# Kernel tuning notes

Measured on AMD Instinct MI355X. Metric: run time of the kernel, lower is better.

The kernel has to match this reference:

```python
import jax, jax.numpy as jnp
import numpy as np

B, N, NODE_DIM = 256, 200, 2
H, D, L, FF = 8, 128, 3, 512
KD = D // H  # key/val dim per head = 16
EPS = 1e-5


def _uniform(key, shape, fan):
    s = 1.0 / np.sqrt(fan)
    return jax.random.uniform(key, shape, jnp.float32, -s, s)


def setup_inputs() -> dict:
    key = jax.random.key(0)
    ks = jax.random.split(key, 16)
    return {
        "x": jax.random.normal(ks[0], (B, N, NODE_DIM), jnp.float32),
        "Wemb": _uniform(ks[1], (NODE_DIM, D), NODE_DIM),
        "bemb": _uniform(ks[2], (D,), NODE_DIM),
        "Wq": _uniform(ks[3], (L, H, D, KD), KD),
        "Wk": _uniform(ks[4], (L, H, D, KD), KD),
        "Wv": _uniform(ks[5], (L, H, D, KD), KD),
        "Wo": _uniform(ks[6], (L, H, KD, D), D),
        "bn1_g": jnp.ones((L, D), jnp.float32),
        "bn1_b": jnp.zeros((L, D), jnp.float32),
        "W1": _uniform(ks[7], (L, D, FF), D),
        "b1": _uniform(ks[8], (L, FF), D),
        "W2": _uniform(ks[9], (L, FF, D), FF),
        "b2": _uniform(ks[10], (L, D), FF),
        "bn2_g": jnp.ones((L, D), jnp.float32),
        "bn2_b": jnp.zeros((L, D), jnp.float32),
    }


def _batch_norm(h, g, b):
    # BatchNorm1d in training mode: stats over all (batch*graph) positions per channel
    hf = h.reshape(-1, h.shape[-1])
    m = hf.mean(axis=0)
    v = hf.var(axis=0)  # biased variance, as torch uses for normalization
    return (h - m) * jax.lax.rsqrt(v + EPS) * g + b


def _mha(h, Wq, Wk, Wv, Wo):
    # h: [B,N,D]; Wq/Wk/Wv: [H,D,KD]; Wo: [H,KD,D]
    Q = jnp.einsum('bnd,hdk->hbnk', h, Wq)
    K = jnp.einsum('bnd,hdk->hbnk', h, Wk)
    V = jnp.einsum('bnd,hdk->hbnk', h, Wv)
    scores = jnp.einsum('hbqk,hbnk->hbqn', Q, K) * (1.0 / np.sqrt(KD))
    attn = jax.nn.softmax(scores, axis=-1)
    heads = jnp.einsum('hbqn,hbnk->hbqk', attn, V)
    return jnp.einsum('hbqk,hkd->bqd', heads, Wo)


def reference(x, Wemb, bemb, Wq, Wk, Wv, Wo, bn1_g, bn1_b, W1, b1, W2, b2, bn2_g, bn2_b):
    h = x @ Wemb + bemb  # init_embed: [B,N,D]
    for l in range(L):
        h = h + _mha(h, Wq[l], Wk[l], Wv[l], Wo[l])
        h = _batch_norm(h, bn1_g[l], bn1_b[l])
        ff = jax.nn.relu(h @ W1[l] + b1[l]) @ W2[l] + b2[l]
        h = _batch_norm(h + ff, bn2_g[l], bn2_b[l])
    return (h, h.mean(axis=1))
```

## Files before the change

kernel.cpp:

```cpp
#include <hip/hip_runtime.h>
#include <math.h>

#define B_ 256
#define N_ 200
#define D_ 128
#define H_ 8
#define KD_ 16
#define L_ 3
#define FF_ 512
#define ROWS (B_*N_)
#define BND (ROWS*D_)

typedef float f32x4 __attribute__((ext_vector_type(4)));
typedef _Float16 f16x4 __attribute__((ext_vector_type(4)));
typedef _Float16 f16x8 __attribute__((ext_vector_type(8)));

__device__ __forceinline__ ushort f2h_bits(float f) {
  _Float16 h = (_Float16)f;
  union { _Float16 h; ushort u; } v; v.h = h; return v.u;
}
__device__ __forceinline__ float h2f(ushort u) {
  union { ushort u; _Float16 h; } v; v.u = u; return (float)v.h;
}
__device__ __forceinline__ void splith(float f, ushort& hi, ushort& lo) {
  _Float16 h = (_Float16)f;
  float hf = (float)h;
  _Float16 l = (_Float16)(f - hf);
  union { _Float16 h; ushort u; } a, b; a.h = h; b.h = l;
  hi = a.u; lo = b.u;
}
__device__ __forceinline__ void bn_reduce(const float* psum, const float* psq,
    const float* gamma, const float* beta, int c, float& sc, float& sh) {
  if (gamma == nullptr) { sc = 1.f; sh = 0.f; return; }
  float s = 0.f, q = 0.f;
  for (int r = 0; r < 400; r++) { s += psum[r*128 + c]; q += psq[r*128 + c]; }
  const float invM = 1.f / 51200.f;
  float m = s * invM;
  float v = fmaf(q, invM, -m * m);
  float rr = rsqrtf(v + 1e-5f);
  sc = rr * gamma[c];
  sh = fmaf(-m, sc, beta[c]);
}

__global__ __launch_bounds__(256) void embed_kernel(const float* __restrict__ x,
    const float* __restrict__ Wemb, const float* __restrict__ bemb,
    ushort* __restrict__ hhi, ushort* __restrict__ hlo)
{
  int i4 = blockIdx.x * 256 + threadIdx.x;
  int r  = i4 >> 5, c4 = i4 & 31;
  float x0 = x[2*r], x1 = x[2*r + 1];
  const float4 w0 = ((const float4*)Wemb)[c4];
  const float4 w1 = ((const float4*)Wemb)[32 + c4];
  const float4 bb = ((const float4*)bemb)[c4];
  float o[4];
  o[0] = fmaf(x0, w0.x, fmaf(x1, w1.x, bb.x));
  o[1] = fmaf(x0, w0.y, fmaf(x1, w1.y, bb.y));
  o[2] = fmaf(x0, w0.z, fmaf(x1, w1.z, bb.z));
  o[3] = fmaf(x0, w0.w, fmaf(x1, w1.w, bb.w));
  ushort hi[4], lo[4];
#pragma unroll
  for (int k = 0; k < 4; k++) splith(o[k], hi[k], lo[k]);
  uint2 ph, pl;
  ph.x = (uint)hi[0] | ((uint)hi[1] << 16);
  ph.y = (uint)hi[2] | ((uint)hi[3] << 16);
  pl.x = (uint)lo[0] | ((uint)lo[1] << 16);
  pl.y = (uint)lo[2] | ((uint)lo[3] << 16);
  ((uint2*)hhi)[i4] = ph;
  ((uint2*)hlo)[i4] = pl;
}

__global__ __launch_bounds__(256) void t_weights(const float* __restrict__ Wo,
    const float* __restrict__ W2, ushort* __restrict__ woT, ushort* __restrict__ w2T)
{
  int i = blockIdx.x * 256 + threadIdx.x;
  if (i < 49152) {
    int l = i / 16384, r = i % 16384;
    int n = r >> 7, k = r & 127;
    int hh = k >> 4, kd = k & 15;
    woT[i] = f2h_bits(Wo[l*16384 + hh*2048 + kd*128 + n]);
  } else {
    int j = i - 49152;
    int l = j / 65536, r = j % 65536;
    int d = r >> 9, f = r & 511;
    w2T[j] = f2h_bits(W2[l*65536 + f*128 + d]);
  }
}

__global__ __launch_bounds__(128) void fold_qkv(const float* __restrict__ Wq,
    const float* __restrict__ Wk, const float* __restrict__ Wv,
    const float* __restrict__ psum, const float* __restrict__ psq,
    const float* __restrict__ gamma, const float* __restrict__ beta,
    ushort* __restrict__ wh, float* __restrict__ bout,
    float* __restrict__ scout, float* __restrict__ shout)
{
  __shared__ float wsum[2];
  int n = blockIdx.x;
  int k = threadIdx.x;
  float sc, sh;
  bn_reduce(psum, psq, gamma, beta, k, sc, sh);
  if (n == 0) { scout[k] = sc; shout[k] = sh; }
  int which = n >> 7, hh = (n >> 4) & 7, kd = n & 15;
  const float* src = (which == 0) ? Wq : (which == 1) ? Wk : Wv;
  float w = src[hh*2048 + k*16 + kd];
  if (which == 0) w *= 0.25f * 1.44269504088896340736f;
  wh[n*128 + k] = f2h_bits(w * sc);
  float p = sh * w;
#pragma unroll
  for (int d = 1; d < 64; d <<= 1) p += __shfl_xor(p, d);
  if ((k & 63) == 0) wsum[k >> 6] = p;
  __syncthreads();
  if (k == 0) bout[n] = wsum[0] + wsum[1];
}

__global__ __launch_bounds__(128) void fold_w1(const float* __restrict__ W1,
    const float* __restrict__ b1,
    const float* __restrict__ psum, const float* __restrict__ psq,
    const float* __restrict__ gamma, const float* __restrict__ beta,
    ushort* __restrict__ wh, float* __restrict__ bout,
    float* __restrict__ scout, float* __restrict__ shout)
{
  __shared__ float wsum[2];
  int f = blockIdx.x;
  int k = threadIdx.x;
  float sc, sh;
  bn_reduce(psum, psq, gamma, beta, k, sc, sh);
  if (f == 0) { scout[k] = sc; shout[k] = sh; }
  float w = W1[k*512 + f];
  wh[f*128 + k] = f2h_bits(w * sc);
  float p = sh * w;
#pragma unroll
  for (int d = 1; d < 64; d <<= 1) p += __shfl_xor(p, d);
  if ((k & 63) == 0) wsum[k >> 6] = p;
  __syncthreads();
  if (k == 0) bout[f] = b1[f] + wsum[0] + wsum[1];
}

template<int K, bool BIAS, bool RELU, bool RESIDBN,
         bool OUTQKV, bool OUT16, bool OUTHL, bool STATS>
__global__ __launch_bounds__(256, 2) void gemm_mfma(
    const ushort* __restrict__ Ah,
    const ushort* __restrict__ Wh,
    const float* __restrict__ bias,
    const ushort* rhi, const ushort* rlo,
    const float* __restrict__ rsc, const float* __restrict__ rsh,
    ushort* o0, ushort* o1, ushort* o2,
    float* __restrict__ psum, float* __restrict__ psq, int Ntot)
{
  __shared__ ushort AhS[128*64];
  __shared__ ushort BhS[128*64];
  const int t    = threadIdx.x;
  const int nx   = gridDim.x;
  const int nwg  = nx * gridDim.y;
  const int lin  = blockIdx.y * nx + blockIdx.x;
  const int q8   = nwg >> 3, r8 = nwg & 7;
  const int xcd  = lin & 7, i8 = lin >> 3;
  const int wg   = (xcd < r8 ? xcd*(q8+1) : r8*(q8+1) + (xcd-r8)*q8) + i8;
  const int bm   = (wg / nx) * 128;
  const int bn   = (wg % nx) * 128;
  const int lane = t & 63;
  const int w    = t >> 6, wm = w >> 1, wn = w & 1;
  const int quad = lane >> 4, l15 = lane & 15;
  const int bky  = wg / nx;

  f32x4 acc[4][4];
#pragma unroll
  for (int i = 0; i < 4; i++)
#pragma unroll
    for (int j = 0; j < 4; j++) acc[i][j] = (f32x4){0.f, 0.f, 0.f, 0.f};

  const ushort* AhB = Ah + (size_t)bm * K;
  const ushort* BhB = Wh + (size_t)bn * K;

  for (int k0 = 0; k0 < K; k0 += 64) {
#pragma unroll
    for (int i = 0; i < 4; i++) {
      int idx = i * 256 + t;
      int row = idx >> 3, c = idx & 7;
      int k8  = c ^ (row & 7);
      size_t off = (size_t)row * K + k0 + k8 * 8;
      ((uint4*)AhS)[idx] = *(const uint4*)(AhB + off);
      ((uint4*)BhS)[idx] = *(const uint4*)(BhB + off);
    }
    __syncthreads();
#pragma unroll
    for (int ks = 0; ks < 2; ks++) {
      f16x8 ah[4], bh[4];
#pragma unroll
      for (int i = 0; i < 4; i++) {
        int row = wm * 64 + i * 16 + l15;
        int k8  = ks * 4 + quad;
        int ci  = k8 ^ (row & 7);
        ah[i] = ((const f16x8*)AhS)[row * 8 + ci];
        int nrow = wn * 64 + i * 16 + l15;
        int cj   = k8 ^ (nrow & 7);
        bh[i] = ((const f16x8*)BhS)[nrow * 8 + cj];
      }
#pragma unroll
      for (int i = 0; i < 4; i++)
#pragma unroll
        for (int j = 0; j < 4; j++)
          acc[i][j] = __builtin_amdgcn_mfma_f32_16x16x32_f16(ah[i], bh[j], acc[i][j], 0, 0, 0);
    }
    __syncthreads();
  }

  float bv[4], scv[4], shv[4];
#pragma unroll
  for (int j = 0; j < 4; j++) {
    int col = bn + wn*64 + j*16 + l15;
    if (BIAS)    bv[j]  = bias[col];
    if (RESIDBN) { scv[j] = rsc[col]; shv[j] = rsh[col]; }
  }
  float sj[4] = {0.f,0.f,0.f,0.f}, qj[4] = {0.f,0.f,0.f,0.f};
#pragma unroll
  for (int i = 0; i < 4; i++) {
#pragma unroll
    for (int r = 0; r < 4; r++) {
      int row = bm + wm*64 + i*16 + quad*4 + r;
#pragma unroll
      for (int j = 0; j < 4; j++) {
        int col = bn + wn*64 + j*16 + l15;
        float v = acc[i][j][r];
        if (BIAS)    v += bv[j];
        if (RELU)    v = fmaxf(v, 0.f);
        if (RESIDBN) {
          size_t ri = (size_t)row * Ntot + col;
          float rr = h2f(rhi[ri]) + h2f(rlo[ri]);
          v += fmaf(rr, scv[j], shv[j]);
        }
        if (OUTQKV) {
          if (bn == 0) {
            o0[((size_t)(col >> 4) * ROWS + row) * 16 + (col & 15)] = f2h_bits(v);
          } else if (bn == 128) {
            int c = col - 128;
            o1[((size_t)(c >> 4) * ROWS + row) * 16 + (c & 15)] = f2h_bits(v);
          } else {
            int c = col - 256;
            o2[((size_t)(c >> 4) * ROWS + row) * 16 + (c & 15)] = f2h_bits(v);
          }
        }
        if (OUT16) o0[(size_t)row * Ntot + col] = f2h_bits(v);
        if (OUTHL) {
          ushort hi, lo; splith(v, hi, lo);
          o0[(size_t)row * Ntot + col] = hi;
          o1[(size_t)row * Ntot + col] = lo;
        }
        if (STATS) { sj[j] += v; qj[j] = fmaf(v, v, qj[j]); }
      }
    }
  }
  if (STATS) {
#pragma unroll
    for (int j = 0; j < 4; j++) {
      sj[j] += __shfl_xor(sj[j], 16); sj[j] += __shfl_xor(sj[j], 32);
      qj[j] += __shfl_xor(qj[j], 16); qj[j] += __shfl_xor(qj[j], 32);
    }
    float* ssum = (float*)AhS;
    float* ssq  = ssum + 128;
    if (t < 128) { ssum[t] = 0.f; ssq[t] = 0.f; }
    __syncthreads();
    if (quad == 0) {
#pragma unroll
      for (int j = 0; j < 4; j++) {
        int col = wn*64 + j*16 + l15;
        atomicAdd(&ssum[col], sj[j]);
        atomicAdd(&ssq[col],  qj[j]);
      }
    }
    __syncthreads();
    if (t < 128) {
      psum[bky * 128 + t] = ssum[t];
      psq [bky * 128 + t] = ssq[t];
    }
  }
}

__global__ __launch_bounds__(256) void attn_kernel(const ushort* __restrict__ qs,
    const ushort* __restrict__ ks, const ushort* __restrict__ vh,
    ushort* __restrict__ hd)
{
  __shared__ __align__(16) _Float16 Ksh[208*24];
  __shared__ __align__(16) _Float16 VTh[16*216];
  const int b  = blockIdx.x >> 3;
  const int hh = blockIdx.x & 7;
  const int t  = threadIdx.x;
  const size_t rb = (size_t)b * N_;
  const size_t hb = ((size_t)hh * ROWS + rb) * 16;

  for (int i = t; i < 208*2; i += 256) {
    int n = i >> 1, half = i & 1;
    uint4 kv = {0u, 0u, 0u, 0u};
    if (n < N_) kv = *(const uint4*)(ks + hb + n*16 + half*8);
    *(uint4*)&Ksh[n*24 + half*8] = kv;
  }
  for (int i = t; i < 208*2; i += 256) {
    int n = i >> 1, half = i & 1;
    uint4 v0 = {0u, 0u, 0u, 0u};
    if (n < N_) v0 = *(const uint4*)(vh + hb + n*16 + half*8);
    const ushort* e0 = (const ushort*)&v0;
#pragma unroll
    for (int q = 0; q < 8; q++)
      ((ushort*)VTh)[(half*8 + q)*216 + n] = e0[q];
  }
  __syncthreads();

  const int lane = t & 63;
  const int w    = t >> 6;
  const int l15  = lane & 15;
  const int g    = lane >> 4;

  for (int qt = w; qt < 13; qt += 4) {
    int qr  = qt*16 + l15;
    int qrc = qr < N_ ? qr : N_-1;
    f16x4 bq = *(const f16x4*)(qs + hb + (size_t)qrc*16 + g*4);

    f32x4 ct[13];
#pragma unroll
    for (int kt = 0; kt < 13; kt++) {
      f16x4 ak = *(const f16x4*)&Ksh[(kt*16 + l15)*24 + g*4];
      ct[kt] = __builtin_amdgcn_mfma_f32_16x16x16f16(ak, bq, (f32x4){0.f,0.f,0.f,0.f}, 0, 0, 0);
    }
#pragma unroll
    for (int r = 0; r < 4; r++)
      if (g*4 + r >= 8) ct[12][r] = -1e30f;

    float m0 = -1e30f, m1 = -1e30f;
#pragma unroll
    for (int kt = 0; kt < 13; kt++) {
      m0 = fmaxf(m0, fmaxf(ct[kt][0], ct[kt][1]));
      m1 = fmaxf(m1, fmaxf(ct[kt][2], ct[kt][3]));
    }
    float m = fmaxf(m0, m1);
    m = fmaxf(m, __shfl_xor(m, 16));
    m = fmaxf(m, __shfl_xor(m, 32));

    float la0 = 0.f, la1 = 0.f, la2 = 0.f, la3 = 0.f;
#pragma unroll
    for (int kt = 0; kt < 13; kt++) {
      float p0 = __builtin_amdgcn_exp2f(ct[kt][0] - m);
      float p1 = __builtin_amdgcn_exp2f(ct[kt][1] - m);
      float p2 = __builtin_amdgcn_exp2f(ct[kt][2] - m);
      float p3 = __builtin_amdgcn_exp2f(ct[kt][3] - m);
      la0 += p0; la1 += p1; la2 += p2; la3 += p3;
      ct[kt][0] = p0; ct[kt][1] = p1; ct[kt][2] = p2; ct[kt][3] = p3;
    }
    float l = (la0 + la1) + (la2 + la3);
    l += __shfl_xor(l, 16);
    l += __shfl_xor(l, 32);

    f32x4 och = {0.f,0.f,0.f,0.f};
#pragma unroll
    for (int kt = 0; kt < 13; kt++) {
      f16x4 pt = { (_Float16)ct[kt][0], (_Float16)ct[kt][1],
                   (_Float16)ct[kt][2], (_Float16)ct[kt][3] };
      f16x4 avh = *(const f16x4*)&VTh[l15*216 + kt*16 + g*4];
      och = __builtin_amdgcn_mfma_f32_16x16x16f16(avh, pt, och, 0, 0, 0);
    }

    if (qr < N_) {
      float inv = __builtin_amdgcn_rcpf(l);
      ushort o16[4];
#pragma unroll
      for (int r = 0; r < 4; r++) o16[r] = f2h_bits(och[r] * inv);
      uint2 p;
      p.x = (uint)o16[0] | ((uint)o16[1] << 16);
      p.y = (uint)o16[2] | ((uint)o16[3] << 16);
      *(uint2*)(hd + (rb + qr)*128 + hh*16 + g*4) = p;
    }
  }
}

__global__ __launch_bounds__(256) void bn_mean_final(const ushort* __restrict__ hhi,
    const ushort* __restrict__ hlo,
    const float* __restrict__ psum, const float* __restrict__ psq,
    const float* __restrict__ gamma, const float* __restrict__ beta,
    float* __restrict__ outh, float* __restrict__ mout)
{
  __shared__ float part[2][128];
  int b = blockIdx.x;
  int t = threadIdx.x;
  int d = t & 127, half = t >> 7;
  float sc, sh;
  bn_reduce(psum, psq, gamma, beta, d, sc, sh);
  float s = 0.f;
  for (int n = half*100; n < half*100 + 100; n++) {
    size_t idx = ((size_t)b * N_ + n) * 128 + d;
    float v = fmaf(h2f(hhi[idx]) + h2f(hlo[idx]), sc, sh);
    outh[idx] = v;
    s += v;
  }
  part[half][d] = s;
  __syncthreads();
  if (half == 0) mout[b * 128 + d] = (part[0][d] + part[1][d]) * (1.f / N_);
}

extern "C" void kernel_launch(void* const* d_in, const int* in_sizes, int n_in,
                              void* d_out, int out_size, void* d_ws, size_t ws_size,
                              hipStream_t stream)
{
  const float* x    = (const float*)d_in[0];
  const float* Wemb = (const float*)d_in[1];
  const float* bemb = (const float*)d_in[2];
  const float* Wq   = (const float*)d_in[3];
  const float* Wk   = (const float*)d_in[4];
  const float* Wv   = (const float*)d_in[5];
  const float* Wo   = (const float*)d_in[6];
  const float* bn1g = (const float*)d_in[7];
  const float* bn1b = (const float*)d_in[8];
  const float* W1   = (const float*)d_in[9];
  const float* b1   = (const float*)d_in[10];
  const float* W2   = (const float*)d_in[11];
  const float* b2   = (const float*)d_in[12];
  const float* bn2g = (const float*)d_in[13];
  const float* bn2b = (const float*)d_in[14];
  float* out = (float*)d_out;

  char* wsb = (char*)d_ws;
  ushort* h_hi  = (ushort*)wsb;
  ushort* h_lo  = (ushort*)(wsb + 13107200);
  char*   phase = wsb + 26214400;
  ushort* qsb   = (ushort*)phase;
  ushort* ksb   = (ushort*)(phase + 13107200);
  ushort* vhh   = (ushort*)(phase + 26214400);
  ushort* hd    = (ushort*)(phase + 52428800);
  ushort* hid   = (ushort*)phase;
  char*   wp    = wsb + 91750400;
  ushort* woT   = (ushort*)wp;
  ushort* w2T   = (ushort*)(wp + 98304);
  ushort* fqkvw = (ushort*)(wp + 491520);
  ushort* fw1w  = (ushort*)(wp + 589824);
  float*  fqkv_b = (float*)(wp + 720896);
  float*  fw1_b  = (float*)(wp + 722432);
  float*  psum   = (float*)(wp + 724480);
  float*  psq    = (float*)(wp + 929280);
  float*  sc_a   = (float*)(wp + 1134080);
  float*  sh_a   = (float*)(wp + 1134592);
  float*  sc_b   = (float*)(wp + 1135104);
  float*  sh_b   = (float*)(wp + 1135616);

  embed_kernel<<<6400, 256, 0, stream>>>(x, Wemb, bemb, h_hi, h_lo);
  t_weights<<<960, 256, 0, stream>>>(Wo, W2, woT, w2T);

  for (int l = 0; l < L_; l++) {
    fold_qkv<<<384, 128, 0, stream>>>(Wq + l*16384, Wk + l*16384, Wv + l*16384,
                                      psum, psq,
                                      l == 0 ? nullptr : bn2g + (l-1)*128,
                                      l == 0 ? nullptr : bn2b + (l-1)*128,
                                      fqkvw, fqkv_b, sc_b, sh_b);
    gemm_mfma<128, true, false, false, true, false, false, false>
        <<<dim3(3, 400), 256, 0, stream>>>(
        h_hi, fqkvw, fqkv_b, nullptr, nullptr, nullptr, nullptr,
        qsb, ksb, vhh, nullptr, nullptr, 384);
    attn_kernel<<<B_ * H_, 256, 0, stream>>>(qsb, ksb, vhh, hd);
    gemm_mfma<128, false, false, true, false, false, true, true>
        <<<dim3(1, 400), 256, 0, stream>>>(
        hd, woT + l*16384, nullptr, h_hi, h_lo, sc_b, sh_b,
        h_hi, h_lo, nullptr, psum, psq, 128);
    fold_w1<<<512, 128, 0, stream>>>(W1 + l*65536, b1 + l*512,
                                     psum, psq, bn1g + l*128, bn1b + l*128,
                                     fw1w, fw1_b, sc_a, sh_a);
    gemm_mfma<128, true, true, false, false, true, false, false>
        <<<dim3(4, 400), 256, 0, stream>>>(
        h_hi, fw1w, fw1_b, nullptr, nullptr, nullptr, nullptr,
        hid, nullptr, nullptr, nullptr, nullptr, 512);
    gemm_mfma<512, true, false, true, false, false, true, true>
        <<<dim3(1, 400), 256, 0, stream>>>(
        hid, w2T + l*65536, b2 + l*128, h_hi, h_lo, sc_a, sh_a,
        h_hi, h_lo, nullptr, psum, psq, 128);
  }

  bn_mean_final<<<B_, 256, 0, stream>>>(h_hi, h_lo, psum, psq,
                                        bn2g + 2*128, bn2b + 2*128, out, out + BND);
}
```

Before: 596.9 us.

## Store hidden state in single fp16, atomic BN stats, merge init kernels

```diff
diff --git a/kernel.cpp b/kernel.cpp
--- a/kernel.cpp
+++ b/kernel.cpp
@@ -22,18 +22,10 @@
 __device__ __forceinline__ float h2f(ushort u) {
   union { ushort u; _Float16 h; } v; v.u = u; return (float)v.h;
 }
-__device__ __forceinline__ void splith(float f, ushort& hi, ushort& lo) {
-  _Float16 h = (_Float16)f;
-  float hf = (float)h;
-  _Float16 l = (_Float16)(f - hf);
-  union { _Float16 h; ushort u; } a, b; a.h = h; b.h = l;
-  hi = a.u; lo = b.u;
-}
 __device__ __forceinline__ void bn_reduce(const float* psum, const float* psq,
     const float* gamma, const float* beta, int c, float& sc, float& sh) {
   if (gamma == nullptr) { sc = 1.f; sh = 0.f; return; }
-  float s = 0.f, q = 0.f;
-  for (int r = 0; r < 400; r++) { s += psum[r*128 + c]; q += psq[r*128 + c]; }
+  float s = psum[c], q = psq[c];
   const float invM = 1.f / 51200.f;
   float m = s * invM;
   float v = fmaf(q, invM, -m * m);
@@ -42,63 +34,63 @@
   sh = fmaf(-m, sc, beta[c]);
 }
 
-__global__ __launch_bounds__(256) void embed_kernel(const float* __restrict__ x,
+__global__ __launch_bounds__(256) void init_kernel(const float* __restrict__ x,
     const float* __restrict__ Wemb, const float* __restrict__ bemb,
-    ushort* __restrict__ hhi, ushort* __restrict__ hlo)
-{
-  int i4 = blockIdx.x * 256 + threadIdx.x;
-  int r  = i4 >> 5, c4 = i4 & 31;
-  float x0 = x[2*r], x1 = x[2*r + 1];
-  const float4 w0 = ((const float4*)Wemb)[c4];
-  const float4 w1 = ((const float4*)Wemb)[32 + c4];
-  const float4 bb = ((const float4*)bemb)[c4];
-  float o[4];
-  o[0] = fmaf(x0, w0.x, fmaf(x1, w1.x, bb.x));
-  o[1] = fmaf(x0, w0.y, fmaf(x1, w1.y, bb.y));
-  o[2] = fmaf(x0, w0.z, fmaf(x1, w1.z, bb.z));
-  o[3] = fmaf(x0, w0.w, fmaf(x1, w1.w, bb.w));
-  ushort hi[4], lo[4];
-#pragma unroll
-  for (int k = 0; k < 4; k++) splith(o[k], hi[k], lo[k]);
-  uint2 ph, pl;
-  ph.x = (uint)hi[0] | ((uint)hi[1] << 16);
-  ph.y = (uint)hi[2] | ((uint)hi[3] << 16);
-  pl.x = (uint)lo[0] | ((uint)lo[1] << 16);
-  pl.y = (uint)lo[2] | ((uint)lo[3] << 16);
-  ((uint2*)hhi)[i4] = ph;
-  ((uint2*)hlo)[i4] = pl;
-}
-
-__global__ __launch_bounds__(256) void t_weights(const float* __restrict__ Wo,
-    const float* __restrict__ W2, ushort* __restrict__ woT, ushort* __restrict__ w2T)
-{
-  int i = blockIdx.x * 256 + threadIdx.x;
-  if (i < 49152) {
-    int l = i / 16384, r = i % 16384;
-    int n = r >> 7, k = r & 127;
-    int hh = k >> 4, kd = k & 15;
-    woT[i] = f2h_bits(Wo[l*16384 + hh*2048 + kd*128 + n]);
+    const float* __restrict__ Wo, const float* __restrict__ W2,
+    ushort* __restrict__ h, ushort* __restrict__ woT, ushort* __restrict__ w2T,
+    float* __restrict__ pa_s, float* __restrict__ pa_q,
+    float* __restrict__ pb_s, float* __restrict__ pb_q)
+{
+  int blk = blockIdx.x, t = threadIdx.x;
+  if (blk < 6400) {
+    int i4 = blk * 256 + t;
+    int r  = i4 >> 5, c4 = i4 & 31;
+    float x0 = x[2*r], x1 = x[2*r + 1];
+    const float4 w0 = ((const float4*)Wemb)[c4];
+    const float4 w1 = ((const float4*)Wemb)[32 + c4];
+    const float4 bb = ((const float4*)bemb)[c4];
+    ushort o16[4];
+    o16[0] = f2h_bits(fmaf(x0, w0.x, fmaf(x1, w1.x, bb.x)));
+    o16[1] = f2h_bits(fmaf(x0, w0.y, fmaf(x1, w1.y, bb.y)));
+    o16[2] = f2h_bits(fmaf(x0, w0.z, fmaf(x1, w1.z, bb.z)));
+    o16[3] = f2h_bits(fmaf(x0, w0.w, fmaf(x1, w1.w, bb.w)));
+    uint2 p;
+    p.x = (uint)o16[0] | ((uint)o16[1] << 16);
+    p.y = (uint)o16[2] | ((uint)o16[3] << 16);
+    ((uint2*)h)[i4] = p;
+  } else if (blk < 7360) {
+    int i = (blk - 6400) * 256 + t;
+    if (i < 49152) {
+      int l = i / 16384, r = i % 16384;
+      int n = r >> 7, k = r & 127;
+      int hh = k >> 4, kd = k & 15;
+      woT[i] = f2h_bits(Wo[l*16384 + hh*2048 + kd*128 + n]);
+    } else {
+      int j = i - 49152;
+      int l = j / 65536, r = j % 65536;
+      int d = r >> 9, f = r & 511;
+      w2T[j] = f2h_bits(W2[l*65536 + f*128 + d]);
+    }
   } else {
-    int j = i - 49152;
-    int l = j / 65536, r = j % 65536;
-    int d = r >> 9, f = r & 511;
-    w2T[j] = f2h_bits(W2[l*65536 + f*128 + d]);
+    if (t < 128) { pa_s[t] = 0.f; pa_q[t] = 0.f; pb_s[t] = 0.f; pb_q[t] = 0.f; }
   }
 }
 
 __global__ __launch_bounds__(128) void fold_qkv(const float* __restrict__ Wq,
     const float* __restrict__ Wk, const float* __restrict__ Wv,
-    const float* __restrict__ psum, const float* __restrict__ psq,
+    const float* __restrict__ pb_s, const float* __restrict__ pb_q,
     const float* __restrict__ gamma, const float* __restrict__ beta,
     ushort* __restrict__ wh, float* __restrict__ bout,
-    float* __restrict__ scout, float* __restrict__ shout)
+    float* __restrict__ scout, float* __restrict__ shout,
+    float* __restrict__ pa_s, float* __restrict__ pa_q)
 {
   __shared__ float wsum[2];
   int n = blockIdx.x;
   int k = threadIdx.x;
   float sc, sh;
-  bn_reduce(psum, psq, gamma, beta, k, sc, sh);
+  bn_reduce(pb_s, pb_q, gamma, beta, k, sc, sh);
   if (n == 0) { scout[k] = sc; shout[k] = sh; }
+  if (n == 1) { pa_s[k] = 0.f; pa_q[k] = 0.f; }
   int which = n >> 7, hh = (n >> 4) & 7, kd = n & 15;
   const float* src = (which == 0) ? Wq : (which == 1) ? Wk : Wv;
   float w = src[hh*2048 + k*16 + kd];
@@ -114,7 +106,7 @@
 
 __global__ __launch_bounds__(128) void fold_w1(const float* __restrict__ W1,
     const float* __restrict__ b1,
-    const float* __restrict__ psum, const float* __restrict__ psq,
+    const float* __restrict__ pa_s, const float* __restrict__ pa_q,
     const float* __restrict__ gamma, const float* __restrict__ beta,
     ushort* __restrict__ wh, float* __restrict__ bout,
     float* __restrict__ scout, float* __restrict__ shout)
@@ -123,7 +115,7 @@
   int f = blockIdx.x;
   int k = threadIdx.x;
   float sc, sh;
-  bn_reduce(psum, psq, gamma, beta, k, sc, sh);
+  bn_reduce(pa_s, pa_q, gamma, beta, k, sc, sh);
   if (f == 0) { scout[k] = sc; shout[k] = sh; }
   float w = W1[k*512 + f];
   wh[f*128 + k] = f2h_bits(w * sc);
@@ -136,12 +128,12 @@
 }
 
 template<int K, bool BIAS, bool RELU, bool RESIDBN,
-         bool OUTQKV, bool OUT16, bool OUTHL, bool STATS>
+         bool OUTQKV, bool OUT16, bool STATS>
 __global__ __launch_bounds__(256, 2) void gemm_mfma(
     const ushort* __restrict__ Ah,
     const ushort* __restrict__ Wh,
     const float* __restrict__ bias,
-    const ushort* rhi, const ushort* rlo,
+    const ushort* rh,
     const float* __restrict__ rsc, const float* __restrict__ rsh,
     ushort* o0, ushort* o1, ushort* o2,
     float* __restrict__ psum, float* __restrict__ psq, int Ntot)
@@ -160,7 +152,6 @@
   const int lane = t & 63;
   const int w    = t >> 6, wm = w >> 1, wn = w & 1;
   const int quad = lane >> 4, l15 = lane & 15;
-  const int bky  = wg / nx;
 
   f32x4 acc[4][4];
 #pragma unroll
@@ -224,8 +215,7 @@
         if (BIAS)    v += bv[j];
         if (RELU)    v = fmaxf(v, 0.f);
         if (RESIDBN) {
-          size_t ri = (size_t)row * Ntot + col;
-          float rr = h2f(rhi[ri]) + h2f(rlo[ri]);
+          float rr = h2f(rh[(size_t)row * Ntot + col]);
           v += fmaf(rr, scv[j], shv[j]);
         }
         if (OUTQKV) {
@@ -240,11 +230,6 @@
           }
         }
         if (OUT16) o0[(size_t)row * Ntot + col] = f2h_bits(v);
-        if (OUTHL) {
-          ushort hi, lo; splith(v, hi, lo);
-          o0[(size_t)row * Ntot + col] = hi;
-          o1[(size_t)row * Ntot + col] = lo;
-        }
         if (STATS) { sj[j] += v; qj[j] = fmaf(v, v, qj[j]); }
       }
     }
@@ -269,21 +254,22 @@
     }
     __syncthreads();
     if (t < 128) {
-      psum[bky * 128 + t] = ssum[t];
-      psq [bky * 128 + t] = ssq[t];
+      atomicAdd(&psum[t], ssum[t]);
+      atomicAdd(&psq[t],  ssq[t]);
     }
   }
 }
 
 __global__ __launch_bounds__(256) void attn_kernel(const ushort* __restrict__ qs,
     const ushort* __restrict__ ks, const ushort* __restrict__ vh,
-    ushort* __restrict__ hd)
+    ushort* __restrict__ hd, float* __restrict__ pb_s, float* __restrict__ pb_q)
 {
   __shared__ __align__(16) _Float16 Ksh[208*24];
   __shared__ __align__(16) _Float16 VTh[16*216];
   const int b  = blockIdx.x >> 3;
   const int hh = blockIdx.x & 7;
   const int t  = threadIdx.x;
+  if (blockIdx.x == 0 && t < 128) { pb_s[t] = 0.f; pb_q[t] = 0.f; }
   const size_t rb = (size_t)b * N_;
   const size_t hb = ((size_t)hh * ROWS + rb) * 16;
 
@@ -370,9 +356,8 @@
   }
 }
 
-__global__ __launch_bounds__(256) void bn_mean_final(const ushort* __restrict__ hhi,
-    const ushort* __restrict__ hlo,
-    const float* __restrict__ psum, const float* __restrict__ psq,
+__global__ __launch_bounds__(256) void bn_mean_final(const ushort* __restrict__ h,
+    const float* __restrict__ pb_s, const float* __restrict__ pb_q,
     const float* __restrict__ gamma, const float* __restrict__ beta,
     float* __restrict__ outh, float* __restrict__ mout)
 {
@@ -381,11 +366,11 @@
   int t = threadIdx.x;
   int d = t & 127, half = t >> 7;
   float sc, sh;
-  bn_reduce(psum, psq, gamma, beta, d, sc, sh);
+  bn_reduce(pb_s, pb_q, gamma, beta, d, sc, sh);
   float s = 0.f;
   for (int n = half*100; n < half*100 + 100; n++) {
     size_t idx = ((size_t)b * N_ + n) * 128 + d;
-    float v = fmaf(h2f(hhi[idx]) + h2f(hlo[idx]), sc, sh);
+    float v = fmaf(h2f(h[idx]), sc, sh);
     outh[idx] = v;
     s += v;
   }
@@ -416,59 +401,60 @@
   float* out = (float*)d_out;
 
   char* wsb = (char*)d_ws;
-  ushort* h_hi  = (ushort*)wsb;
-  ushort* h_lo  = (ushort*)(wsb + 13107200);
-  char*   phase = wsb + 26214400;
+  ushort* h     = (ushort*)wsb;
+  char*   phase = wsb + 13107200;
   ushort* qsb   = (ushort*)phase;
   ushort* ksb   = (ushort*)(phase + 13107200);
   ushort* vhh   = (ushort*)(phase + 26214400);
   ushort* hd    = (ushort*)(phase + 52428800);
   ushort* hid   = (ushort*)phase;
-  char*   wp    = wsb + 91750400;
+  char*   wp    = wsb + 78643200;
   ushort* woT   = (ushort*)wp;
   ushort* w2T   = (ushort*)(wp + 98304);
   ushort* fqkvw = (ushort*)(wp + 491520);
   ushort* fw1w  = (ushort*)(wp + 589824);
   float*  fqkv_b = (float*)(wp + 720896);
   float*  fw1_b  = (float*)(wp + 722432);
-  float*  psum   = (float*)(wp + 724480);
-  float*  psq    = (float*)(wp + 929280);
-  float*  sc_a   = (float*)(wp + 1134080);
-  float*  sh_a   = (float*)(wp + 1134592);
-  float*  sc_b   = (float*)(wp + 1135104);
-  float*  sh_b   = (float*)(wp + 1135616);
-
-  embed_kernel<<<6400, 256, 0, stream>>>(x, Wemb, bemb, h_hi, h_lo);
-  t_weights<<<960, 256, 0, stream>>>(Wo, W2, woT, w2T);
+  float*  pa_s   = (float*)(wp + 724480);
+  float*  pa_q   = (float*)(wp + 724992);
+  float*  pb_s   = (float*)(wp + 725504);
+  float*  pb_q   = (float*)(wp + 726016);
+  float*  sc_a   = (float*)(wp + 726528);
+  float*  sh_a   = (float*)(wp + 727040);
+  float*  sc_b   = (float*)(wp + 727552);
+  float*  sh_b   = (float*)(wp + 728064);
+
+  init_kernel<<<7361, 256, 0, stream>>>(x, Wemb, bemb, Wo, W2, h, woT, w2T,
+                                        pa_s, pa_q, pb_s, pb_q);
 
   for (int l = 0; l < L_; l++) {
     fold_qkv<<<384, 128, 0, stream>>>(Wq + l*16384, Wk + l*16384, Wv + l*16384,
-                                      psum, psq,
+                                      pb_s, pb_q,
                                       l == 0 ? nullptr : bn2g + (l-1)*128,
                                       l == 0 ? nullptr : bn2b + (l-1)*128,
-                                      fqkvw, fqkv_b, sc_b, sh_b);
-    gemm_mfma<128, true, false, false, true, false, false, false>
+                                      fqkvw, fqkv_b, sc_b, sh_b, pa_s, pa_q);
+    gemm_mfma<128, true, false, false, true, false, false>
         <<<dim3(3, 400), 256, 0, stream>>>(
-        h_hi, fqkvw, fqkv_b, nullptr, nullptr, nullptr, nullptr,
+        h, fqkvw, fqkv_b, nullptr, nullptr, nullptr,
         qsb, ksb, vhh, nullptr, nullptr, 384);
-    attn_kernel<<<B_ * H_, 256, 0, stream>>>(qsb, ksb, vhh, hd);
-    gemm_mfma<128, false, false, true, false, false, true, true>
+    attn_kernel<<<B_ * H_, 256, 0, stream>>>(qsb, ksb, vhh, hd, pb_s, pb_q);
+    gemm_mfma<128, false, false, true, false, true, true>
         <<<dim3(1, 400), 256, 0, stream>>>(
-        hd, woT + l*16384, nullptr, h_hi, h_lo, sc_b, sh_b,
-        h_hi, h_lo, nullptr, psum, psq, 128);
+        hd, woT + l*16384, nullptr, h, sc_b, sh_b,
+        h, nullptr, nullptr, pa_s, pa_q, 128);
     fold_w1<<<512, 128, 0, stream>>>(W1 + l*65536, b1 + l*512,
-                                     psum, psq, bn1g + l*128, bn1b + l*128,
+                                     pa_s, pa_q, bn1g + l*128, bn1b + l*128,
                                      fw1w, fw1_b, sc_a, sh_a);
-    gemm_mfma<128, true, true, false, false, true, false, false>
+    gemm_mfma<128, true, true, false, false, true, false>
         <<<dim3(4, 400), 256, 0, stream>>>(
-        h_hi, fw1w, fw1_b, nullptr, nullptr, nullptr, nullptr,
+        h, fw1w, fw1_b, nullptr, nullptr, nullptr,
         hid, nullptr, nullptr, nullptr, nullptr, 512);
-    gemm_mfma<512, true, false, true, false, false, true, true>
+    gemm_mfma<512, true, false, true, false, true, true>
         <<<dim3(1, 400), 256, 0, stream>>>(
-        hid, w2T + l*65536, b2 + l*128, h_hi, h_lo, sc_a, sh_a,
-        h_hi, h_lo, nullptr, psum, psq, 128);
-  }
-
-  bn_mean_final<<<B_, 256, 0, stream>>>(h_hi, h_lo, psum, psq,
+        hid, w2T + l*65536, b2 + l*128, h, sc_a, sh_a,
+        h, nullptr, nullptr, pb_s, pb_q, 128);
+  }
+
+  bn_mean_final<<<B_, 256, 0, stream>>>(h, pb_s, pb_q,
                                         bn2g + 2*128, bn2b + 2*128, out, out + BND);
 }
```

After: 527.7 us. 1.13x faster.
